# Optimization experiments

Measured on AMD Instinct MI355X. Metric: run time of the kernel, lower is better.

The kernel has to match this reference:

```python
import jax, jax.numpy as jnp
import numpy as np

BETA = 0.25
N_CODEBOOK = 2  # hard-coded in the original module
EPS = 1e-12     # torch F.normalize default eps


def l2norm(t):
    # matches torch.nn.functional.normalize(t, p=2, dim=-1)
    n = jnp.linalg.norm(t, axis=-1, keepdims=True)
    return t / jnp.maximum(n, EPS)


def setup_inputs() -> dict:
    key = jax.random.key(0)
    k1, k2 = jax.random.split(key)
    b, n, e_dim, n_e = 16, 256, 1024, 4096
    c = e_dim // N_CODEBOOK
    z = jax.random.normal(k1, (b, n, e_dim), dtype=jnp.float32)
    emb_weight = jax.random.normal(k2, (N_CODEBOOK * n_e, c), dtype=jnp.float32)
    return {"z": z, "emb_weight": emb_weight}


def reference(z, emb_weight):
    b, n, e_dim = z.shape
    f = N_CODEBOOK
    c = e_dim // f
    n_e = emb_weight.shape[0] // f

    # 'b n (f c) -> b f n c'
    zf = jnp.transpose(z.reshape(b, n, f, c), (0, 2, 1, 3))
    # '(b f) c -> b f c' with b=2 (codebooks), f=n_e
    protos = emb_weight.reshape(f, n_e, c)

    zn = l2norm(zf)            # (b, f, n, c)
    pn = l2norm(protos)        # (f, m, c)

    # cosine distance; batch repeat of prototypes is a pure broadcast
    d = 2.0 - 2.0 * jnp.einsum('bfnc,fmc->bfnm', zn, pn)  # (b, f, n, m)
    encoding_indices = jnp.argmin(d, axis=-1)              # (b, f, n) in [0, n_e)

    # faithful to source: indices gather from the FULL (2*n_e) table, no offset
    z_q = l2norm(emb_weight[encoding_indices])             # (b, f, n, c)

    sg = jax.lax.stop_gradient
    loss = BETA * jnp.mean((sg(z_q) - zn) ** 2) + jnp.mean((z_q - sg(zn)) ** 2)

    z_q_st = zn + sg(z_q - zn)                             # straight-through
    # 'b f n c -> b n (f c)'
    z_q_out = jnp.transpose(z_q_st, (0, 2, 1, 3)).reshape(b, n, e_dim)
    return z_q_out, loss, encoding_indices
```

## Files before the change

kernel.cpp:

```cpp
#include <hip/hip_runtime.h>
#include <hip/hip_bf16.h>
#include <stdint.h>

#define FCB 2
#define BB 16
#define NN 256
#define EDIM 1024
#define CC 512
#define NE 4096
#define TOKENS (BB*FCB*NN)
#define ROWS (FCB*NE)
#define OUT_LOSS (BB*NN*EDIM)
#define OUT_IDX  (OUT_LOSS + 1)
#define MARGIN 0.15f

typedef __attribute__((ext_vector_type(8))) short bf16x8;
typedef __attribute__((ext_vector_type(4))) float f32x4;

__device__ __forceinline__ unsigned int ford(float v) {
    unsigned int u = __float_as_uint(v);
    return (u & 0x80000000u) ? ~u : (u | 0x80000000u);
}
__device__ __forceinline__ float unford(unsigned int u) {
    unsigned int b = (u & 0x80000000u) ? (u & 0x7fffffffu) : ~u;
    return __uint_as_float(b);
}


__global__ __launch_bounds__(256) void pack_hi(
    const float* __restrict__ z, const float* __restrict__ emb,
    short* __restrict__ z_hi, short* __restrict__ e_hi,
    float* __restrict__ norm_sq)
{
    __shared__ float red[256];
    int bid = blockIdx.x;
    int tid = threadIdx.x;
    bool is_emb = (bid >= 2048);
    const float* src; short* hi; int RS, FRO, FCO;
    if (!is_emb) { src = z;   hi = z_hi; RS = EDIM; FRO = 0;  FCO = CC; }
    else         { src = emb; hi = e_hi; RS = CC;   FRO = NE; FCO = 0; bid -= 2048; }
    int u = bid * 256 + tid;
    int m = u & 15;
    int Q = (u >> 4) & 63;
    int R = (u >> 10) & 255;
    int f = u >> 18;
    int row = R * 16 + m;
    const float* s = src + (size_t)(f * FRO + row) * RS + f * FCO + Q * 8;
    float4 v0 = *(const float4*)s;
    float4 v1 = *(const float4*)(s + 4);
    float vv[8] = {v0.x, v0.y, v0.z, v0.w, v1.x, v1.y, v1.z, v1.w};
    bf16x8 h8;
    float ss = 0.f;
    #pragma unroll
    for (int j = 0; j < 8; ++j) {
        __hip_bfloat16 hb = __float2bfloat16(vv[j]);
        h8[j] = *(short*)&hb;
        ss = fmaf(vv[j], vv[j], ss);
    }
    *(bf16x8*)(hi + (size_t)u * 8) = h8;

    if (is_emb) {
        red[tid] = ss;
        __syncthreads();
        if (tid < 16) {
            float t = 0.f;
            #pragma unroll
            for (int q = 0; q < 16; ++q) t += red[tid + 16 * q];
            int bf = (bid * 256) >> 18;
            int bR = ((bid * 256) >> 10) & 255;
            atomicAdd(norm_sq + bf * NE + bR * 16 + tid, t);
        }
    }
}

__global__ __launch_bounds__(256, 2) void gemm_sel(
    const short* __restrict__ zh, const short* __restrict__ eh,
    const float* __restrict__ norm_sq, unsigned int* __restrict__ cand)
{
    __shared__ __attribute__((aligned(128))) char smem[2][32768];
    const int f  = blockIdx.z;
    const int t0 = blockIdx.y * 128;
    const int m0 = blockIdx.x * 128;
    const int tid  = threadIdx.x;
    const int wave = tid >> 6, lane = tid & 63;
    const int wm = wave & 1, wn = wave >> 1;

    f32x4 acc[4][4] = {};

    auto stage = [&](int step, char* dst) {
        #pragma unroll
        for (int i = 0; i < 8; ++i) {
            int c = wave * 8 + i;
            const short* gsrc = (c < 16) ? zh : eh;
            int cl = c & 15;
            int Rl = cl >> 1, h = cl & 1;
            int R = ((c < 16) ? (t0 >> 4) : (m0 >> 4)) + Rl;
            int qb = step * 8 + h * 4;
            const short* g = gsrc
                + (((size_t)f * 256 + R) * 64 + qb) * 128 + (size_t)lane * 8;
            __builtin_amdgcn_global_load_lds(
                (const __attribute__((address_space(1))) void*)g,
                (__attribute__((address_space(3))) void*)(dst + c * 1024),
                16, 0, 0);
        }
    };

    stage(0, smem[0]);
    __syncthreads();

    #pragma unroll
    for (int step = 0; step < 8; ++step) {
        const char* cur = smem[step & 1];
        if (step < 7) stage(step + 1, smem[(step & 1) ^ 1]);

        #pragma unroll
        for (int h = 0; h < 2; ++h) {
            bf16x8 ah[4], bh[4];
            #pragma unroll
            for (int i = 0; i < 4; ++i) {
                ah[i] = *(const bf16x8*)(cur + ((wm*4 + i)*2 + h) * 1024 + lane * 16);
                bh[i] = *(const bf16x8*)(cur + 16384 + ((wn*4 + i)*2 + h) * 1024 + lane * 16);
            }
            #pragma unroll
            for (int i = 0; i < 4; ++i)
                #pragma unroll
                for (int j2 = 0; j2 < 4; ++j2)
                    acc[i][j2] = __builtin_amdgcn_mfma_f32_16x16x32_bf16(ah[i], bh[j2], acc[i][j2], 0, 0, 0);
        }
        __syncthreads();
    }

    float inm[4]; unsigned ccode[4];
    #pragma unroll
    for (int j2 = 0; j2 < 4; ++j2) {
        int col = j2 * 16 + (lane & 15);
        ccode[j2] = (unsigned)(col ^ 63);
        inm[j2] = rsqrtf(norm_sq[f * NE + m0 + wn * 64 + col]);
    }

    #pragma unroll
    for (int i = 0; i < 4; ++i) {
        #pragma unroll
        for (int r = 0; r < 4; ++r) {
            unsigned p1 = 0u, p2 = 0u;
            #pragma unroll
            for (int j2 = 0; j2 < 4; ++j2) {
                float w = acc[i][j2][r] * inm[j2];
                unsigned pw = (ford(w) & 0xFFFFFFC0u) | ccode[j2];
                if (pw > p1) { p2 = p1; p1 = pw; }
                else if (pw > p2) p2 = pw;
            }
            #pragma unroll
            for (int off = 8; off; off >>= 1) {
                unsigned q1 = __shfl_down(p1, off, 16);
                unsigned q2 = __shfl_down(p2, off, 16);
                if (q1 > p1) { unsigned t = p1; p1 = q1; p2 = (t > q2) ? t : q2; }
                else         { p2 = (p2 > q1) ? p2 : q1; }
            }
            if ((lane & 15) == 0) {
                int u = t0 + wm * 64 + i * 16 + (lane >> 4) * 4 + r;
                int b = u >> 8, n = u & 255;
                int gt = ((b * FCB + f) << 8) + n;
                int s = (blockIdx.x << 1) | wn;
                uint2 val; val.x = p1; val.y = p2;
                *(uint2*)(cand + ((size_t)gt << 7) + (s << 1)) = val;
            }
        }
    }
}

__global__ __launch_bounds__(256) void rescore_epilogue(
    const float* __restrict__ z, const float* __restrict__ emb,
    const unsigned int* __restrict__ cand, const float* __restrict__ norm_sq,
    float* __restrict__ out, float* __restrict__ loss_tok)
{
    int t = blockIdx.x * 4 + (threadIdx.x >> 6);
    int lane = threadIdx.x & 63;
    int n = t & 255;
    int f = (t >> 8) & 1;
    int b = t >> 9;
    const float* zrow = z + ((size_t)(b*NN + n))*EDIM + f*CC;
    float4 za = *(const float4*)(zrow + lane * 8);
    float4 zb = *(const float4*)(zrow + lane * 8 + 4);

    uint2 cc = *(const uint2*)(cand + ((size_t)t << 7) + (lane << 1));
    unsigned c1 = cc.x, c2 = cc.y;

    unsigned m1 = (c1 > c2) ? c1 : c2;
    #pragma unroll
    for (int off = 32; off; off >>= 1) {
        unsigned o = __shfl_xor(m1, off);
        if (o > m1) m1 = o;
    }
    float thr = unford(m1) - MARGIN;

    unsigned long long bestp = 0ull;
    #pragma unroll
    for (int rnd = 0; rnd < 2; ++rnd) {
        unsigned u = rnd ? c2 : c1;
        float v = unford(u);
        unsigned long long mask = __ballot(v > thr);
        while (mask) {
            int src = __ffsll((long long)mask) - 1;
            mask &= mask - 1;
            unsigned cu = __shfl(u, src);
            int idx = (src << 6) | ((int)(cu & 63u) ^ 63);
            const float* er = emb + ((size_t)(f * NE + idx)) * CC;
            float4 ea = *(const float4*)(er + lane * 8);
            float4 eb = *(const float4*)(er + lane * 8 + 4);
            float d  = za.x*ea.x + za.y*ea.y + za.z*ea.z + za.w*ea.w
                     + zb.x*eb.x + zb.y*eb.y + zb.z*eb.z + zb.w*eb.w;
            #pragma unroll
            for (int off = 32; off; off >>= 1) d += __shfl_xor(d, off);
            float se = norm_sq[f * NE + idx];
            float vex = d / fmaxf(sqrtf(se), 1e-12f);
            unsigned long long pex = ((unsigned long long)ford(vex) << 32)
                                   | (unsigned int)(~(unsigned int)idx);
            if (pex > bestp) bestp = pex;
        }
    }
    int idxb = (int)(~(unsigned int)bestp);

    const float* er0 = emb + (size_t)idxb * CC;
    float4 ea = *(const float4*)(er0 + lane * 8);
    float4 eb = *(const float4*)(er0 + lane * 8 + 4);
    float inm0 = 1.0f / fmaxf(sqrtf(norm_sq[idxb]), 1e-12f);
    float* orow = out + ((size_t)(b*NN + n))*EDIM + f*CC;
    ea.x *= inm0; ea.y *= inm0; ea.z *= inm0; ea.w *= inm0;
    eb.x *= inm0; eb.y *= inm0; eb.z *= inm0; eb.w *= inm0;
    *(float4*)(orow + lane * 8) = ea;
    *(float4*)(orow + lane * 8 + 4) = eb;
    float s1 = za.x*za.x + za.y*za.y + za.z*za.z + za.w*za.w
             + zb.x*zb.x + zb.y*zb.y + zb.z*zb.z + zb.w*zb.w;
    float s2 = za.x*ea.x + za.y*ea.y + za.z*ea.z + za.w*ea.w
             + zb.x*eb.x + zb.y*eb.y + zb.z*eb.z + zb.w*eb.w;
    #pragma unroll
    for (int off = 32; off; off >>= 1) {
        s1 += __shfl_xor(s1, off);
        s2 += __shfl_xor(s2, off);
    }
    if (lane == 0) {
        float cosv = s2 / fmaxf(sqrtf(s1), 1e-12f);
        loss_tok[t] = 2.0f - 2.0f * cosv;
        out[OUT_IDX + t] = (float)idxb;
    }
}

__global__ __launch_bounds__(256) void loss_reduce(
    const float* __restrict__ loss_tok, float* __restrict__ out)
{
    int tid = threadIdx.x;
    float s = 0.f;
    #pragma unroll
    for (int h = 0; h < 32; ++h) s += loss_tok[h * 256 + tid];
    #pragma unroll
    for (int off = 32; off; off >>= 1) s += __shfl_down(s, off);
    __shared__ float part[4];
    if ((tid & 63) == 0) part[tid >> 6] = s;
    __syncthreads();
    if (tid == 0) {
        float t = part[0] + part[1] + part[2] + part[3];
        out[OUT_LOSS] = t * (1.25f / (float)OUT_LOSS);
    }
}

extern "C" void kernel_launch(void* const* d_in, const int* in_sizes, int n_in,
                              void* d_out, int out_size, void* d_ws, size_t ws_size,
                              hipStream_t stream) {
    const float* z   = (const float*)d_in[0];
    const float* emb = (const float*)d_in[1];
    float* out = (float*)d_out;

    char* ws = (char*)d_ws;
    float* norm_sq = (float*)ws;
    unsigned int* cand = (unsigned int*)(ws + 32768);
    float* loss_tok = (float*)(ws + 32768 + (size_t)4*1024*1024);
    short* z_hi = (short*)(ws + 65536 + (size_t)4*1024*1024);
    short* e_hi = z_hi + (size_t)FCB * NE * CC;

    hipMemsetAsync(norm_sq, 0, ROWS * sizeof(float), stream);
    pack_hi<<<4096, 256, 0, stream>>>(z, emb, z_hi, e_hi, norm_sq);
    gemm_sel<<<dim3(NE/128, NE/128, FCB), 256, 0, stream>>>(z_hi, e_hi, norm_sq, cand);
    rescore_epilogue<<<TOKENS/4, 256, 0, stream>>>(z, emb, cand, norm_sq, out, loss_tok);
    loss_reduce<<<1, 256, 0, stream>>>(loss_tok, out);
}
```

Baseline: 149.5 us.

## Single-buffer GEMM LDS, remap workgroups per XCD, compute emb norms without atomics

The pack kernel now has each emb block process one full 16-row group, so squared norms are written directly. This removes the atomics and the preceding memset. The GEMM drops LDS double buffering to a single 32KB buffer and raises the occupancy target to 3 blocks per CU. It also remaps workgroup IDs so each XCD handles a contiguous slice of codebook tiles for better L2 reuse. The cost is that global-to-LDS loads no longer overlap with MFMA work inside a block, leaving latency hiding to the extra occupancy.

```diff
diff --git a/kernel.cpp b/kernel.cpp
--- a/kernel.cpp
+++ b/kernel.cpp
@@ -35,59 +35,79 @@
     __shared__ float red[256];
     int bid = blockIdx.x;
     int tid = threadIdx.x;
-    bool is_emb = (bid >= 2048);
-    const float* src; short* hi; int RS, FRO, FCO;
-    if (!is_emb) { src = z;   hi = z_hi; RS = EDIM; FRO = 0;  FCO = CC; }
-    else         { src = emb; hi = e_hi; RS = CC;   FRO = NE; FCO = 0; bid -= 2048; }
-    int u = bid * 256 + tid;
-    int m = u & 15;
-    int Q = (u >> 4) & 63;
-    int R = (u >> 10) & 255;
-    int f = u >> 18;
-    int row = R * 16 + m;
-    const float* s = src + (size_t)(f * FRO + row) * RS + f * FCO + Q * 8;
-    float4 v0 = *(const float4*)s;
-    float4 v1 = *(const float4*)(s + 4);
-    float vv[8] = {v0.x, v0.y, v0.z, v0.w, v1.x, v1.y, v1.z, v1.w};
-    bf16x8 h8;
-    float ss = 0.f;
-    #pragma unroll
-    for (int j = 0; j < 8; ++j) {
-        __hip_bfloat16 hb = __float2bfloat16(vv[j]);
-        h8[j] = *(short*)&hb;
-        ss = fmaf(vv[j], vv[j], ss);
-    }
-    *(bf16x8*)(hi + (size_t)u * 8) = h8;
-
-    if (is_emb) {
+    if (bid < 2048) {
+        int u = bid * 256 + tid;
+        int m = u & 15;
+        int Q = (u >> 4) & 63;
+        int R = (u >> 10) & 255;
+        int f = u >> 18;
+        int row = R * 16 + m;
+        const float* s = z + (size_t)row * EDIM + f * CC + Q * 8;
+        float4 v0 = *(const float4*)s;
+        float4 v1 = *(const float4*)(s + 4);
+        float vv[8] = {v0.x, v0.y, v0.z, v0.w, v1.x, v1.y, v1.z, v1.w};
+        bf16x8 h8;
+        #pragma unroll
+        for (int j = 0; j < 8; ++j) {
+            __hip_bfloat16 hb = __float2bfloat16(vv[j]);
+            h8[j] = *(short*)&hb;
+        }
+        *(bf16x8*)(z_hi + (size_t)u * 8) = h8;
+    } else {
+        int e = bid - 2048;
+        int f = e >> 8, R = e & 255;
+        int m = tid & 15;
+        float ss = 0.f;
+        #pragma unroll
+        for (int i = 0; i < 4; ++i) {
+            int ul = tid + 256 * i;
+            int Q = (ul >> 4) & 63;
+            const float* s = emb + ((size_t)(f * NE + R * 16 + m)) * CC + Q * 8;
+            float4 v0 = *(const float4*)s;
+            float4 v1 = *(const float4*)(s + 4);
+            float vv[8] = {v0.x, v0.y, v0.z, v0.w, v1.x, v1.y, v1.z, v1.w};
+            bf16x8 h8;
+            #pragma unroll
+            for (int j = 0; j < 8; ++j) {
+                __hip_bfloat16 hb = __float2bfloat16(vv[j]);
+                h8[j] = *(short*)&hb;
+                ss = fmaf(vv[j], vv[j], ss);
+            }
+            int u = ((f * 256 + R) * 64 + Q) * 16 + m;
+            *(bf16x8*)(e_hi + (size_t)u * 8) = h8;
+        }
         red[tid] = ss;
         __syncthreads();
         if (tid < 16) {
             float t = 0.f;
             #pragma unroll
             for (int q = 0; q < 16; ++q) t += red[tid + 16 * q];
-            int bf = (bid * 256) >> 18;
-            int bR = ((bid * 256) >> 10) & 255;
-            atomicAdd(norm_sq + bf * NE + bR * 16 + tid, t);
-        }
-    }
-}
-
-__global__ __launch_bounds__(256, 2) void gemm_sel(
+            norm_sq[f * NE + R * 16 + tid] = t;
+        }
+    }
+}
+
+__global__ __launch_bounds__(256, 3) void gemm_sel(
     const short* __restrict__ zh, const short* __restrict__ eh,
     const float* __restrict__ norm_sq, unsigned int* __restrict__ cand)
 {
-    __shared__ __attribute__((aligned(128))) char smem[2][32768];
-    const int f  = blockIdx.z;
-    const int t0 = blockIdx.y * 128;
-    const int m0 = blockIdx.x * 128;
+    __shared__ char smem[32768];
+    const int wg  = blockIdx.x + 32 * (blockIdx.y + 32 * blockIdx.z);
+    const int xcd   = wg & 7;
+    const int local = wg >> 3;
+    const int t0i = local & 31;
+    const int f   = (local >> 5) & 1;
+    const int m0i = (xcd << 2) | (local >> 6);
+    const int t0 = t0i * 128;
+    const int m0 = m0i * 128;
     const int tid  = threadIdx.x;
     const int wave = tid >> 6, lane = tid & 63;
     const int wm = wave & 1, wn = wave >> 1;
 
     f32x4 acc[4][4] = {};
 
-    auto stage = [&](int step, char* dst) {
+    for (int step = 0; step < 8; ++step) {
+        __syncthreads();
         #pragma unroll
         for (int i = 0; i < 8; ++i) {
             int c = wave * 8 + i;
@@ -100,26 +120,18 @@
                 + (((size_t)f * 256 + R) * 64 + qb) * 128 + (size_t)lane * 8;
             __builtin_amdgcn_global_load_lds(
                 (const __attribute__((address_space(1))) void*)g,
-                (__attribute__((address_space(3))) void*)(dst + c * 1024),
+                (__attribute__((address_space(3))) void*)(smem + c * 1024),
                 16, 0, 0);
         }
-    };
-
-    stage(0, smem[0]);
-    __syncthreads();
-
-    #pragma unroll
-    for (int step = 0; step < 8; ++step) {
-        const char* cur = smem[step & 1];
-        if (step < 7) stage(step + 1, smem[(step & 1) ^ 1]);
+        __syncthreads();
 
         #pragma unroll
         for (int h = 0; h < 2; ++h) {
             bf16x8 ah[4], bh[4];
             #pragma unroll
             for (int i = 0; i < 4; ++i) {
-                ah[i] = *(const bf16x8*)(cur + ((wm*4 + i)*2 + h) * 1024 + lane * 16);
-                bh[i] = *(const bf16x8*)(cur + 16384 + ((wn*4 + i)*2 + h) * 1024 + lane * 16);
+                ah[i] = *(const bf16x8*)(smem + ((wm*4 + i)*2 + h) * 1024 + lane * 16);
+                bh[i] = *(const bf16x8*)(smem + 16384 + ((wn*4 + i)*2 + h) * 1024 + lane * 16);
             }
             #pragma unroll
             for (int i = 0; i < 4; ++i)
@@ -127,7 +139,6 @@
                 for (int j2 = 0; j2 < 4; ++j2)
                     acc[i][j2] = __builtin_amdgcn_mfma_f32_16x16x32_bf16(ah[i], bh[j2], acc[i][j2], 0, 0, 0);
         }
-        __syncthreads();
     }
 
     float inm[4]; unsigned ccode[4];
@@ -161,7 +172,7 @@
                 int u = t0 + wm * 64 + i * 16 + (lane >> 4) * 4 + r;
                 int b = u >> 8, n = u & 255;
                 int gt = ((b * FCB + f) << 8) + n;
-                int s = (blockIdx.x << 1) | wn;
+                int s = (m0i << 1) | wn;
                 uint2 val; val.x = p1; val.y = p2;
                 *(uint2*)(cand + ((size_t)gt << 7) + (s << 1)) = val;
             }
@@ -278,9 +289,8 @@
     short* z_hi = (short*)(ws + 65536 + (size_t)4*1024*1024);
     short* e_hi = z_hi + (size_t)FCB * NE * CC;
 
-    hipMemsetAsync(norm_sq, 0, ROWS * sizeof(float), stream);
-    pack_hi<<<4096, 256, 0, stream>>>(z, emb, z_hi, e_hi, norm_sq);
-    gemm_sel<<<dim3(NE/128, NE/128, FCB), 256, 0, stream>>>(z_hi, e_hi, norm_sq, cand);
+    pack_hi<<<2560, 256, 0, stream>>>(z, emb, z_hi, e_hi, norm_sq);
+    gemm_sel<<<dim3(32, 32, FCB), 256, 0, stream>>>(z_hi, e_hi, norm_sq, cand);
     rescore_epilogue<<<TOKENS/4, 256, 0, stream>>>(z, emb, cand, norm_sq, out, loss_tok);
     loss_reduce<<<1, 256, 0, stream>>>(loss_tok, out);
 }
```

New measurement: 147.6 us. Within noise of the previous version (-1.3%).
